# Kernel tuning notes

Hardware: AMD Instinct MI355X
Metric: run time of the kernel (lower is better)

Reference implementation:

```python
import jax, jax.numpy as jnp
import numpy as np

H, D, BLK, R = 12, 64, 64, 3  # heads, size_per_head, block size, rand blocks
NEG = -1e9


def setup_inputs() -> dict:
    key = jax.random.key(0)
    ks = jax.random.split(key, 6)
    B, S, W = 2, 4096, H * D
    M = S // BLK
    return {
        "from_tensor": jax.random.normal(ks[0], (B, S, W), jnp.float32),
        "to_tensor": jax.random.normal(ks[1], (B, S, W), jnp.float32),
        "Wq": jax.random.normal(ks[2], (W, H * D), jnp.float32) * 0.02,
        "bq": jnp.zeros((H * D,), jnp.float32),
        "Wk": jax.random.normal(ks[3], (W, H * D), jnp.float32) * 0.02,
        "bk": jnp.zeros((H * D,), jnp.float32),
        "Wv": jax.random.normal(ks[4], (W, H * D), jnp.float32) * 0.02,
        "bv": jnp.zeros((H * D,), jnp.float32),
        "to_mask": jnp.ones((B, S), jnp.int32),
        "rand_attn": jax.random.randint(ks[5], (H, M - 2, R), 0, M - 2, jnp.int32),
    }


def _bigbird_block_sparse(from_tensor, to_tensor, Wq, bq, Wk, bk, Wv, bv, to_mask, rand_attn):
    B, S, _ = from_tensor.shape
    M = S // BLK
    scale = 1.0 / np.sqrt(D).astype(np.float32)

    # QKV projections -> [B,H,S,D]
    q = (from_tensor @ Wq + bq).reshape(B, S, H, D).transpose(0, 2, 1, 3)
    k = (to_tensor @ Wk + bk).reshape(B, S, H, D).transpose(0, 2, 1, 3)
    v = (to_tensor @ Wv + bv).reshape(B, S, H, D).transpose(0, 2, 1, 3)

    bq_ = q.reshape(B, H, M, BLK, D)
    bk_ = k.reshape(B, H, M, BLK, D)
    bv_ = v.reshape(B, H, M, BLK, D)

    tm = to_mask.astype(q.dtype)          # [B,S]
    bm = tm.reshape(B, M, BLK)            # [B,M,BLK]

    # gather random key/value blocks per head: [B,H,M-2,R*BLK,D]
    ha = jnp.arange(H)[:, None, None]
    gk = bk_[:, ha, rand_attn].reshape(B, H, M - 2, R * BLK, D)
    gv = bv_[:, ha, rand_attn].reshape(B, H, M - 2, R * BLK, D)
    gm = bm[:, rand_attn].reshape(B, H, M - 2, R * BLK)

    def full_row(qblk):  # first/last query blocks attend to everything
        s = jnp.einsum('bhqd,bhkd->bhqk', qblk, k) * scale + (1 - tm)[:, None, None, :] * NEG
        return jnp.einsum('bhqk,bhkd->bhqd', jax.nn.softmax(s, -1), v)

    def sparse_row(qblk, k_cat, v_cat, m_cat):  # [B,H,BLK,D] x [B,H,L,D]
        s = jnp.einsum('bhqd,bhkd->bhqk', qblk, k_cat) * scale + (1 - m_cat)[:, :, None, :] * NEG
        return jnp.einsum('bhqk,bhkd->bhqd', jax.nn.softmax(s, -1), v_cat)

    c_first = full_row(bq_[:, :, 0])
    c_last = full_row(bq_[:, :, M - 1])

    # second row: blocks [0,1,2,last] + rand
    k2 = jnp.concatenate([bk_[:, :, 0], bk_[:, :, 1], bk_[:, :, 2], bk_[:, :, M - 1], gk[:, :, 0]], axis=2)
    v2 = jnp.concatenate([bv_[:, :, 0], bv_[:, :, 1], bv_[:, :, 2], bv_[:, :, M - 1], gv[:, :, 0]], axis=2)
    m2s = jnp.concatenate([bm[:, 0], bm[:, 1], bm[:, 2], bm[:, M - 1]], axis=-1)
    m2 = jnp.concatenate([jnp.broadcast_to(m2s[:, None], (B, H, 4 * BLK)), gm[:, :, 0]], axis=-1)
    c_second = sparse_row(bq_[:, :, 1], k2, v2, m2)

    # second-to-last row: blocks [0,M-3,M-2,M-1] + rand
    k3 = jnp.concatenate([bk_[:, :, 0], bk_[:, :, M - 3], bk_[:, :, M - 2], bk_[:, :, M - 1], gk[:, :, M - 3]], axis=2)
    v3 = jnp.concatenate([bv_[:, :, 0], bv_[:, :, M - 3], bv_[:, :, M - 2], bv_[:, :, M - 1], gv[:, :, M - 3]], axis=2)
    m3s = jnp.concatenate([bm[:, 0], bm[:, M - 3], bm[:, M - 2], bm[:, M - 1]], axis=-1)
    m3 = jnp.concatenate([jnp.broadcast_to(m3s[:, None], (B, H, 4 * BLK)), gm[:, :, M - 3]], axis=-1)
    c_secondlast = sparse_row(bq_[:, :, M - 2], k3, v3, m3)

    # middle rows 2..M-3: band(prev,self,next) + rand + global first/last blocks
    L = M - 4
    band_k = jnp.concatenate([bk_[:, :, 1:M - 3], bk_[:, :, 2:M - 2], bk_[:, :, 3:M - 1]], axis=3)  # [B,H,L,3BLK,D]
    band_v = jnp.concatenate([bv_[:, :, 1:M - 3], bv_[:, :, 2:M - 2], bv_[:, :, 3:M - 1]], axis=3)
    band_m = jnp.concatenate([bm[:, 1:M - 3], bm[:, 2:M - 2], bm[:, 3:M - 1]], axis=-1)  # [B,L,3BLK]

    k_mid = jnp.concatenate([
        band_k, gk[:, :, 1:M - 3],
        jnp.broadcast_to(bk_[:, :, 0:1], (B, H, L, BLK, D)),
        jnp.broadcast_to(bk_[:, :, M - 1:M], (B, H, L, BLK, D))], axis=3)
    v_mid = jnp.concatenate([
        band_v, gv[:, :, 1:M - 3],
        jnp.broadcast_to(bv_[:, :, 0:1], (B, H, L, BLK, D)),
        jnp.broadcast_to(bv_[:, :, M - 1:M], (B, H, L, BLK, D))], axis=3)
    m_mid = jnp.concatenate([
        jnp.broadcast_to(band_m[:, None], (B, H, L, 3 * BLK)),
        gm[:, :, 1:M - 3],
        jnp.broadcast_to(bm[:, None, None, 0], (B, H, L, BLK)),
        jnp.broadcast_to(bm[:, None, None, M - 1], (B, H, L, BLK))], axis=-1)

    s_mid = jnp.einsum('bhlqd,bhlkd->bhlqk', bq_[:, :, 2:M - 2], k_mid) * scale
    s_mid = s_mid + (1 - m_mid)[:, :, :, None, :] * NEG
    c_mid = jnp.einsum('bhlqk,bhlkd->bhlqd', jax.nn.softmax(s_mid, -1), v_mid)

    ctx = jnp.concatenate([
        c_first[:, :, None], c_second[:, :, None], c_mid,
        c_secondlast[:, :, None], c_last[:, :, None]], axis=2)  # [B,H,M,BLK,D]
    return ctx.reshape(B, H, S, D).transpose(0, 2, 1, 3)  # [B,S,H,D]


def reference(from_tensor, to_tensor, Wq, bq, Wk, bk, Wv, bv, to_mask, rand_attn):
    return _bigbird_block_sparse(from_tensor, to_tensor, Wq, bq, Wk, bk, Wv, bv, to_mask, rand_attn)
```

## Files before the change

kernel.cpp:

```cpp
#include <hip/hip_runtime.h>

typedef __attribute__((ext_vector_type(2))) float f32x2;
typedef __attribute__((ext_vector_type(4))) float f32x4;
typedef __attribute__((ext_vector_type(8))) __bf16 bf16x8;
typedef __attribute__((ext_vector_type(8))) unsigned short u16x8;
typedef __attribute__((ext_vector_type(4))) unsigned short u16x4;

#define LOG2E 1.4426950408889634f

__device__ __forceinline__ unsigned short f2bf(float f) {
  unsigned u = __builtin_bit_cast(unsigned, f);
  u += 0x7fffu + ((u >> 16) & 1u);
  return (unsigned short)(u >> 16);
}

__device__ __forceinline__ unsigned cvtpk(float lo, float hi) {
  unsigned r;
  asm("v_cvt_pk_bf16_f32 %0, %1, %2" : "=v"(r) : "v"(lo), "v"(hi));
  return r;
}

__device__ __forceinline__ f32x2 pkadd(f32x2 a, f32x2 b) {
  f32x2 r;
  asm("v_pk_add_f32 %0, %1, %2" : "=v"(r) : "v"(a), "v"(b));
  return r;
}

__device__ __forceinline__ float fexp2(float x) {
  float r;
  asm("v_exp_f32 %0, %1" : "=v"(r) : "v"(x));
  return r;
}

__device__ __forceinline__ f32x4 mfma16(bf16x8 a, bf16x8 b, f32x4 c) {
  return __builtin_amdgcn_mfma_f32_16x16x32_bf16(a, b, c, 0, 0, 0);
}

__device__ __forceinline__ void gload_lds16(const void* g, void* l) {
  __builtin_amdgcn_global_load_lds(
      (const __attribute__((address_space(1))) void*)g,
      (__attribute__((address_space(3))) void*)l, 16, 0, 0);
}

#define NQK 6291456
#define NX 6291456
#define NW 589824

__global__ __launch_bounds__(256) void prep_kernel(
    const float* __restrict__ Wq, const float* __restrict__ Wk,
    const float* __restrict__ Wv, const float* __restrict__ from_t,
    const float* __restrict__ to_t, unsigned short* __restrict__ Wt,
    unsigned short* __restrict__ xb) {
  __shared__ float tile[64][65];
  const int bid = blockIdx.x;
  const int t = threadIdx.x;
  if (bid < 432) {
    const int z = bid / 144, rest = bid % 144;
    const float* __restrict__ src = (z == 0) ? Wq : (z == 1) ? Wk : Wv;
    unsigned short* __restrict__ dst = Wt + (size_t)z * NW;
    const int k0 = (rest / 12) * 64, n0 = (rest % 12) * 64;
    const int r = t >> 4, c4 = (t & 15) * 4;
#pragma unroll
    for (int p = 0; p < 4; ++p) {
      int rr = r + p * 16;
      f32x4 v = *(const f32x4*)(src + (size_t)(k0 + rr) * 768 + n0 + c4);
#pragma unroll
      for (int j = 0; j < 4; ++j) tile[rr][c4 + j] = v[j];
    }
    __syncthreads();
#pragma unroll
    for (int p = 0; p < 4; ++p) {
      int rn = r + p * 16;
      u16x4 o;
#pragma unroll
      for (int j = 0; j < 4; ++j) o[j] = f2bf(tile[c4 + j][rn]);
      *(u16x4*)(dst + (size_t)(n0 + rn) * 768 + k0 + c4) = o;
    }
  } else {
    const int idx = bid - 432;
    const int y = idx / 3072, xi = idx % 3072;
    const float* __restrict__ src = y ? to_t : from_t;
    unsigned short* __restrict__ dst = xb + (size_t)y * NX;
    const size_t i = ((size_t)xi * 256 + t) * 8;
    f32x4 a = *(const f32x4*)(src + i);
    f32x4 b = *(const f32x4*)(src + i + 4);
    u16x8 o;
#pragma unroll
    for (int j = 0; j < 4; ++j) { o[j] = f2bf(a[j]); o[j + 4] = f2bf(b[j]); }
    *(u16x8*)(dst + i) = o;
  }
}

__global__ __launch_bounds__(256) void qkv_gemm_kernel(
    const unsigned short* __restrict__ Xb, const unsigned short* __restrict__ Wt,
    const float* __restrict__ bq, const float* __restrict__ bk,
    const float* __restrict__ bv, unsigned short* __restrict__ qkvQK,
    unsigned short* __restrict__ vt, int zoff, int cpx) {
  __shared__ unsigned short A_lds[2][8192];
  __shared__ unsigned short B_lds[2][8192];
  const int bid0 = blockIdx.x;
  const int bid = (bid0 & 7) * cpx + (bid0 >> 3);
  const int z = zoff + bid / 384;
  const int rem = bid % 384;
  const int bm = rem / 6, bn = rem % 6;
  const unsigned short* __restrict__ X = Xb + (z ? (size_t)NX : 0);
  const unsigned short* __restrict__ Wz = Wt + (size_t)z * NW;
  const float* __restrict__ bias = (z == 0) ? bq : (z == 1) ? bk : bv;
  const int t = threadIdx.x, lane = t & 63, w = t >> 6;
  const int wm = (w >> 1) * 64, wn = (w & 1) * 64;
  const int l15 = lane & 15, cc = lane >> 4;

  f32x4 acc[4][4];
#pragma unroll
  for (int i = 0; i < 4; ++i)
#pragma unroll
    for (int j = 0; j < 4; ++j) acc[i][j] = (f32x4){0.f, 0.f, 0.f, 0.f};

  const unsigned short* Abase = X + (size_t)bm * 128 * 768;
  const unsigned short* Bbase = Wz + (size_t)bn * 128 * 768;

  auto STAGE = [&](int ks, int bufi) {
#pragma unroll
    for (int p = 0; p < 4; ++p) {
      int wb = p * 4 + w;
      int ch = wb * 64 + lane;
      int r = ch >> 3, sl = ch & 7;
      int g = sl ^ (r & 7);
      gload_lds16(Abase + (size_t)r * 768 + ks * 64 + g * 8,
                  &A_lds[bufi][wb * 512]);
      gload_lds16(Bbase + (size_t)r * 768 + ks * 64 + g * 8,
                  &B_lds[bufi][wb * 512]);
    }
  };

  STAGE(0, 0);

  for (int ks = 0; ks < 12; ++ks) {
    const int cur = ks & 1;
    if (ks < 11) {
      STAGE(ks + 1, cur ^ 1);
      asm volatile("s_waitcnt vmcnt(8)" ::: "memory");
    } else {
      asm volatile("s_waitcnt vmcnt(0)" ::: "memory");
    }
    __builtin_amdgcn_s_barrier();
    __builtin_amdgcn_sched_barrier(0);

    bf16x8 af[4][2], bfr[4][2];
#pragma unroll
    for (int mi = 0; mi < 4; ++mi) {
      int row = wm + mi * 16 + l15;
      const char* rp = (const char*)A_lds[cur] + row * 128;
#pragma unroll
      for (int kk = 0; kk < 2; ++kk)
        af[mi][kk] = *(const bf16x8*)(rp + (((cc + 4 * kk) ^ (row & 7)) << 4));
    }
#pragma unroll
    for (int ni = 0; ni < 4; ++ni) {
      int row = wn + ni * 16 + l15;
      const char* rp = (const char*)B_lds[cur] + row * 128;
#pragma unroll
      for (int kk = 0; kk < 2; ++kk)
        bfr[ni][kk] = *(const bf16x8*)(rp + (((cc + 4 * kk) ^ (row & 7)) << 4));
    }
#pragma unroll
    for (int kk = 0; kk < 2; ++kk)
#pragma unroll
      for (int mi = 0; mi < 4; ++mi)
#pragma unroll
        for (int ni = 0; ni < 4; ++ni)
          acc[mi][ni] = mfma16(af[mi][kk], bfr[ni][kk], acc[mi][ni]);
    asm volatile("s_waitcnt lgkmcnt(0)" ::: "memory");
    __builtin_amdgcn_s_barrier();
  }

  if (z < 2) {
    const float qscale = (z == 0) ? 0.125f * LOG2E : 1.0f;
    unsigned short* __restrict__ dst = qkvQK + (size_t)z * NQK;
#pragma unroll
    for (int ni = 0; ni < 4; ++ni) {
      int gn = bn * 128 + wn + ni * 16 + l15;
      float bv_ = bias[gn];
      int hh = gn >> 6, dd = gn & 63;
#pragma unroll
      for (int mi = 0; mi < 4; ++mi) {
#pragma unroll
        for (int r = 0; r < 4; ++r) {
          int gm = bm * 128 + wm + mi * 16 + cc * 4 + r;
          int bb = gm >> 12, s = gm & 4095;
          float val = (acc[mi][ni][r] + bv_) * qscale;
          dst[((((size_t)bb * 12 + hh) * 4096 + s) * 64) + dd] = f2bf(val);
        }
      }
    }
  } else {
#pragma unroll
    for (int ni = 0; ni < 4; ++ni) {
      int gn = bn * 128 + wn + ni * 16 + l15;
      float bv_ = bias[gn];
      int hh = gn >> 6, dd = gn & 63;
#pragma unroll
      for (int mi = 0; mi < 4; ++mi) {
        int gm0 = bm * 128 + wm + mi * 16 + cc * 4;
        int bb = gm0 >> 12, s0 = gm0 & 4095;
        u16x4 o;
#pragma unroll
        for (int r = 0; r < 4; ++r) o[r] = f2bf(acc[mi][ni][r] + bv_);
        *(u16x4*)(vt + ((size_t)(bb * 12 + hh) * 64 + dd) * 4096 + s0) = o;
      }
    }
  }
}

__global__ __launch_bounds__(256, 4) void attn_kernel(
    const unsigned short* __restrict__ qkvQK, const unsigned short* __restrict__ vt,
    const int* __restrict__ to_mask, const int* __restrict__ rand_attn,
    float* __restrict__ out, float* __restrict__ part_o,
    float* __restrict__ part_ml) {
  __shared__ unsigned short K_lds[2][4096];
  __shared__ unsigned short VT_lds[2][4096];
  __shared__ float penal[8][64];
  __shared__ int blist[8];

  const int bid0 = blockIdx.x;
  const int bid = (bid0 & 7) * 234 + (bid0 >> 3);
  const int bh = bid / 78, r78 = bid % 78;
  const int h = bh % 12, b = bh / 12;
  const int t = threadIdx.x, lane = t & 63, w = t >> 6;
  const int l15 = lane & 15, cc = lane >> 4;

  int m, nblk, chunk = 0;
  bool full;
  if (r78 < 62) {
    full = false;
    m = r78 + 1;
    nblk = (m == 1 || m == 62) ? 7 : 8;
    if (t == 0) {
      const int* rp = rand_attn + ((size_t)h * 62 + (m - 1)) * 3;
      if (m == 1) {
        blist[0] = 0; blist[1] = 1; blist[2] = 2; blist[3] = 63;
        blist[4] = rp[0]; blist[5] = rp[1]; blist[6] = rp[2];
      } else if (m == 62) {
        blist[0] = 0; blist[1] = 61; blist[2] = 62; blist[3] = 63;
        blist[4] = rp[0]; blist[5] = rp[1]; blist[6] = rp[2];
      } else {
        blist[0] = m - 1; blist[1] = m; blist[2] = m + 1;
        blist[3] = rp[0]; blist[4] = rp[1]; blist[5] = rp[2];
        blist[6] = 0; blist[7] = 63;
      }
    }
  } else {
    full = true;
    int fr = r78 - 62;
    chunk = fr & 7;
    m = (fr >> 3) ? 63 : 0;
    nblk = 8;
    if (t < 8) blist[t] = chunk * 8 + t;
  }

  const unsigned short* qp = qkvQK + (((size_t)b * 12 + h) * 4096 + m * 64) * 64;
  const unsigned short* kp = qkvQK + NQK + (((size_t)b * 12 + h) * 4096) * 64;
  const unsigned short* vtp = vt + (((size_t)b * 12 + h) * 64) * 4096;

  int loff[2];
  const unsigned short *kpl[2], *vpl[2];
#pragma unroll
  for (int p = 0; p < 2; ++p) {
    int wb = p * 4 + w;
    int ch = wb * 64 + lane;
    int rr = ch >> 3;
    int g = (ch & 7) ^ (rr & 7);
    loff[p] = wb * 512;
    kpl[p] = kp + rr * 64 + g * 8;
    vpl[p] = vtp + rr * 4096 + g * 8;
  }

  int vaddr[4];
#pragma unroll
  for (int dg = 0; dg < 4; ++dg) {
    int d = dg * 16 + l15;
    vaddr[dg] = d * 128 + ((((cc >> 1) ^ (d & 7)) << 4)) + (cc & 1) * 8;
  }

  bf16x8 aq[2];
  {
    int qrow = w * 16 + l15;
    aq[0] = *(const bf16x8*)(qp + qrow * 64 + cc * 8);
    aq[1] = *(const bf16x8*)(qp + qrow * 64 + 32 + cc * 8);
  }

  float m_run = -INFINITY, l_run = 0.f;
  f32x4 o_acc[4];
#pragma unroll
  for (int dg = 0; dg < 4; ++dg) o_acc[dg] = (f32x4){0.f, 0.f, 0.f, 0.f};

  auto STAGE_K = [&](int kb, int bufi) {
    const size_t ko = (size_t)kb * 4096;
    gload_lds16(kpl[0] + ko, &K_lds[bufi][loff[0]]);
    gload_lds16(kpl[1] + ko, &K_lds[bufi][loff[1]]);
  };
  auto STAGE_V = [&](int kb, int bufi) {
    const size_t vo = (size_t)kb * 64;
    gload_lds16(vpl[0] + vo, &VT_lds[bufi][loff[0]]);
    gload_lds16(vpl[1] + vo, &VT_lds[bufi][loff[1]]);
  };

  auto QK = [&](int bufi, int slot, float s[4][4]) {
    const char* kbase = (const char*)K_lds[bufi];
    __builtin_amdgcn_s_setprio(1);
#pragma unroll
    for (int kg = 0; kg < 4; ++kg) {
      int krow = kg * 16 + l15;
      const char* rp = kbase + krow * 128;
      int sz = (krow & 7) << 4;
      bf16x8 k0 = *(const bf16x8*)(rp + ((cc << 4) ^ sz));
      bf16x8 k1 = *(const bf16x8*)(rp + (((cc + 4) << 4) ^ sz));
      f32x4 pen = *(const f32x4*)(&penal[slot][kg * 16 + cc * 4]);
      f32x4 zz = mfma16(k0, aq[0], pen);
      zz = mfma16(k1, aq[1], zz);
#pragma unroll
      for (int r = 0; r < 4; ++r) s[kg][r] = zz[r];
    }
    __builtin_amdgcn_s_setprio(0);
  };

  __syncthreads();

  {
    int ib = w;
#pragma unroll
    for (int pp = 0; pp < 2; ++pp, ib += 4)
      if (ib < nblk)
        penal[ib][lane] =
            (1.0f - (float)to_mask[(size_t)b * 4096 + blist[ib] * 64 + lane]) *
            (-1e9f * LOG2E);
  }
  STAGE_K(blist[0], 0);
  STAGE_V(blist[0], 0);
  STAGE_K(blist[1], 1);
  asm volatile("s_waitcnt vmcnt(4) lgkmcnt(0)" ::: "memory");
  __builtin_amdgcn_s_barrier();
  __builtin_amdgcn_sched_barrier(0);

  float sm[4][4];
  QK(0, 0, sm);

  union PF { unsigned u[4]; bf16x8 v; };
  union VF { u16x4 h2[2]; bf16x8 v; };

  for (int ib = 0; ib < nblk; ++ib) {
    asm volatile("s_waitcnt vmcnt(0)" ::: "memory");
    __builtin_amdgcn_s_barrier();
    __builtin_amdgcn_sched_barrier(0);

    if (ib + 2 < nblk) STAGE_K(blist[ib + 2], ib & 1);
    if (ib + 1 < nblk) STAGE_V(blist[ib + 1], (ib + 1) & 1);

    float sn[4][4];
    if (ib + 1 < nblk) QK((ib + 1) & 1, ib + 1, sn);

    float m1 = fmaxf(fmaxf(sm[0][0], sm[0][1]), sm[0][2]);
    float m2 = fmaxf(fmaxf(sm[0][3], sm[1][0]), sm[1][1]);
    float m3 = fmaxf(fmaxf(sm[1][2], sm[1][3]), sm[2][0]);
    float m4 = fmaxf(fmaxf(sm[2][1], sm[2][2]), sm[2][3]);
    float m5 = fmaxf(fmaxf(sm[3][0], sm[3][1]), sm[3][2]);
    float mx = fmaxf(fmaxf(fmaxf(m1, m2), m3),
                     fmaxf(fmaxf(m4, m5), sm[3][3]));
    mx = fmaxf(mx, __shfl_xor(mx, 16, 64));
    mx = fmaxf(mx, __shfl_xor(mx, 32, 64));

    if (!__all(mx - m_run <= 8.0f)) {
      float mn = fmaxf(m_run, mx);
      float fac = fexp2(m_run - mn);
      m_run = mn;
      l_run *= fac;
      float fr_[4];
#pragma unroll
      for (int r = 0; r < 4; ++r) fr_[r] = __shfl(fac, cc * 4 + r, 64);
#pragma unroll
      for (int dg = 0; dg < 4; ++dg)
#pragma unroll
        for (int r = 0; r < 4; ++r) o_acc[dg][r] *= fr_[r];
    }

    unsigned pk[8];
    f32x2 ps[8];
#pragma unroll
    for (int kg = 0; kg < 4; ++kg) {
      float p0 = fexp2(sm[kg][0] - m_run), p1 = fexp2(sm[kg][1] - m_run);
      float p2 = fexp2(sm[kg][2] - m_run), p3 = fexp2(sm[kg][3] - m_run);
      pk[kg * 2] = cvtpk(p0, p1);
      pk[kg * 2 + 1] = cvtpk(p2, p3);
      ps[kg * 2] = (f32x2){p0, p1};
      ps[kg * 2 + 1] = (f32x2){p2, p3};
    }
    f32x2 s0 = pkadd(pkadd(ps[0], ps[1]), pkadd(ps[2], ps[3]));
    f32x2 s1 = pkadd(pkadd(ps[4], ps[5]), pkadd(ps[6], ps[7]));
    f32x2 st = pkadd(s0, s1);
    float rs = st[0] + st[1];
    rs += __shfl_xor(rs, 16, 64);
    rs += __shfl_xor(rs, 32, 64);
    l_run += rs;

    PF a0, a1;
    a0.u[0] = pk[0]; a0.u[1] = pk[1]; a0.u[2] = pk[2]; a0.u[3] = pk[3];
    a1.u[0] = pk[4]; a1.u[1] = pk[5]; a1.u[2] = pk[6]; a1.u[3] = pk[7];

    const char* vbuf = (const char*)VT_lds[ib & 1];
    __builtin_amdgcn_s_setprio(1);
#pragma unroll
    for (int dg = 0; dg < 4; ++dg) {
      int a00 = vaddr[dg];
      VF f0, f1;
      f0.h2[0] = *(const u16x4*)(vbuf + a00);
      f0.h2[1] = *(const u16x4*)(vbuf + (a00 ^ 32));
      f1.h2[0] = *(const u16x4*)(vbuf + (a00 ^ 64));
      f1.h2[1] = *(const u16x4*)(vbuf + (a00 ^ 96));
      o_acc[dg] = mfma16(a0.v, f0.v, o_acc[dg]);
      o_acc[dg] = mfma16(a1.v, f1.v, o_acc[dg]);
    }
    __builtin_amdgcn_s_setprio(0);

    if (ib + 1 < nblk) {
#pragma unroll
      for (int kg = 0; kg < 4; ++kg)
#pragma unroll
        for (int r = 0; r < 4; ++r) sm[kg][r] = sn[kg][r];
    }
  }

  if (!full) {
    float inv[4];
#pragma unroll
    for (int r = 0; r < 4; ++r) inv[r] = 1.0f / __shfl(l_run, cc * 4 + r, 64);
#pragma unroll
    for (int r = 0; r < 4; ++r) {
      int s = m * 64 + w * 16 + cc * 4 + r;
#pragma unroll
      for (int dg = 0; dg < 4; ++dg) {
        int d = dg * 16 + l15;
        out[(((size_t)b * 4096 + s) * 12 + h) * 64 + d] = o_acc[dg][r] * inv[r];
      }
    }
  } else {
    const int row = (b * 12 + h) * 2 + (m ? 1 : 0);
    float* po = part_o + (((size_t)row * 8 + chunk) * 64) * 64;
    float* pml = part_ml + ((size_t)row * 8 + chunk) * 128;
#pragma unroll
    for (int r = 0; r < 4; ++r) {
      int q = w * 16 + cc * 4 + r;
#pragma unroll
      for (int dg = 0; dg < 4; ++dg) {
        int d = dg * 16 + l15;
        po[q * 64 + d] = o_acc[dg][r];
      }
    }
    if (cc == 0) {
      pml[w * 16 + l15] = m_run;
      pml[64 + w * 16 + l15] = l_run;
    }
  }
}

__global__ __launch_bounds__(256) void combine_kernel(
    const float* __restrict__ part_o, const float* __restrict__ part_ml,
    float* __restrict__ out) {
  const int row = blockIdx.x;
  const int b = row / 24, h = (row >> 1) % 12, m = (row & 1) ? 63 : 0;
  const int t = threadIdx.x;
  const int q = t >> 2, d0 = (t & 3) * 16;

  float mc[8], lc[8];
  float M = -INFINITY;
#pragma unroll
  for (int c = 0; c < 8; ++c) {
    const float* pml = part_ml + ((size_t)row * 8 + c) * 128;
    mc[c] = pml[q];
    lc[c] = pml[64 + q];
    M = fmaxf(M, mc[c]);
  }
  float wgt[8], L = 0.f;
#pragma unroll
  for (int c = 0; c < 8; ++c) {
    float r;
    asm("v_exp_f32 %0, %1" : "=v"(r) : "v"(mc[c] - M));
    wgt[c] = r;
    L += wgt[c] * lc[c];
  }
  f32x4 acc[4];
#pragma unroll
  for (int j = 0; j < 4; ++j) acc[j] = (f32x4){0.f, 0.f, 0.f, 0.f};
#pragma unroll
  for (int c = 0; c < 8; ++c) {
    const float* po = part_o + (((size_t)row * 8 + c) * 64 + q) * 64 + d0;
#pragma unroll
    for (int j = 0; j < 4; ++j) {
      f32x4 v = *(const f32x4*)(po + j * 4);
#pragma unroll
      for (int e = 0; e < 4; ++e) acc[j][e] += wgt[c] * v[e];
    }
  }
  const float inv = 1.0f / L;
  const int s = m * 64 + q;
  float* op = out + (((size_t)b * 4096 + s) * 12 + h) * 64 + d0;
#pragma unroll
  for (int j = 0; j < 4; ++j) {
    f32x4 v;
#pragma unroll
    for (int e = 0; e < 4; ++e) v[e] = acc[j][e] * inv;
    *(f32x4*)(op + j * 4) = v;
  }
}

extern "C" void kernel_launch(void* const* d_in, const int* in_sizes, int n_in,
                              void* d_out, int out_size, void* d_ws,
                              size_t ws_size, hipStream_t stream) {
  (void)in_sizes; (void)n_in; (void)out_size;
  const float* from_t = (const float*)d_in[0];
  const float* to_t = (const float*)d_in[1];
  const float* Wq = (const float*)d_in[2];
  const float* bq = (const float*)d_in[3];
  const float* Wk = (const float*)d_in[4];
  const float* bk = (const float*)d_in[5];
  const float* Wv = (const float*)d_in[6];
  const float* bv = (const float*)d_in[7];
  const int* to_mask = (const int*)d_in[8];
  const int* rand_attn = (const int*)d_in[9];
  float* out = (float*)d_out;

  unsigned short* Wt = (unsigned short*)d_ws;
  unsigned short* qkvQK = Wt + (size_t)3 * NW;
  unsigned short* Xb = qkvQK + (size_t)2 * NQK;

  const size_t part_elems = (size_t)48 * 8 * 64 * 64 + (size_t)48 * 8 * 128;
  const size_t fused_bytes =
      ((size_t)3 * NW + 2 * NQK + 2 * NX + NQK) * 2 + part_elems * 4;

  if (ws_size >= fused_bytes) {
    unsigned short* vt = Xb + (size_t)2 * NX;
    float* part_o = (float*)Xb;
    float* part_ml = part_o + (size_t)48 * 8 * 64 * 64;

    prep_kernel<<<dim3(6576), dim3(256), 0, stream>>>(Wq, Wk, Wv, from_t, to_t,
                                                      Wt, Xb);
    qkv_gemm_kernel<<<dim3(1152), dim3(256), 0, stream>>>(
        Xb, Wt, bq, bk, bv, qkvQK, vt, 0, 144);
    attn_kernel<<<dim3(1872), dim3(256), 0, stream>>>(
        qkvQK, vt, to_mask, rand_attn, out, part_o, part_ml);
    combine_kernel<<<dim3(48), dim3(256), 0, stream>>>(part_o, part_ml, out);
  } else {
    unsigned short* vt = Xb;
    float* part_o = (float*)(Xb + (size_t)NX);
    float* part_ml = part_o + (size_t)48 * 8 * 64 * 64;

    prep_kernel<<<dim3(6576), dim3(256), 0, stream>>>(Wq, Wk, Wv, from_t, to_t,
                                                      Wt, Xb);
    qkv_gemm_kernel<<<dim3(768), dim3(256), 0, stream>>>(
        Xb, Wt, bq, bk, bv, qkvQK, vt, 0, 96);
    qkv_gemm_kernel<<<dim3(384), dim3(256), 0, stream>>>(
        Xb, Wt, bq, bk, bv, qkvQK, vt, 2, 48);
    attn_kernel<<<dim3(1872), dim3(256), 0, stream>>>(
        qkvQK, vt, to_mask, rand_attn, out, part_o, part_ml);
    combine_kernel<<<dim3(48), dim3(256), 0, stream>>>(part_o, part_ml, out);
  }
}
```

Before: 101.7 us.

## Fuse fp32-to-bf16 activation conversion into QKV GEMM A-tile loading

The separate prep pass that converted from/to tensors to bf16 in workspace is removed. The GEMM now loads fp32 activation rows into registers, converts them with packed bf16 conversion and writes them swizzled into LDS, while B tiles still use direct global-to-LDS loads. This removes a full write and re-read of the bf16 activation copies and drops the two-launch fallback path. In exchange, the GEMM reads twice as many bytes for A per tile, uses more registers and needs a more complex wait schedule.

```diff
diff --git a/kernel.cpp b/kernel.cpp
--- a/kernel.cpp
+++ b/kernel.cpp
@@ -5,6 +5,7 @@
 typedef __attribute__((ext_vector_type(8))) __bf16 bf16x8;
 typedef __attribute__((ext_vector_type(8))) unsigned short u16x8;
 typedef __attribute__((ext_vector_type(4))) unsigned short u16x4;
+typedef __attribute__((ext_vector_type(4))) unsigned int u32x4;
 
 #define LOG2E 1.4426950408889634f
 
@@ -43,67 +44,51 @@
 }
 
 #define NQK 6291456
-#define NX 6291456
 #define NW 589824
 
 __global__ __launch_bounds__(256) void prep_kernel(
     const float* __restrict__ Wq, const float* __restrict__ Wk,
-    const float* __restrict__ Wv, const float* __restrict__ from_t,
-    const float* __restrict__ to_t, unsigned short* __restrict__ Wt,
-    unsigned short* __restrict__ xb) {
+    const float* __restrict__ Wv, unsigned short* __restrict__ Wt) {
   __shared__ float tile[64][65];
   const int bid = blockIdx.x;
   const int t = threadIdx.x;
-  if (bid < 432) {
-    const int z = bid / 144, rest = bid % 144;
-    const float* __restrict__ src = (z == 0) ? Wq : (z == 1) ? Wk : Wv;
-    unsigned short* __restrict__ dst = Wt + (size_t)z * NW;
-    const int k0 = (rest / 12) * 64, n0 = (rest % 12) * 64;
-    const int r = t >> 4, c4 = (t & 15) * 4;
-#pragma unroll
-    for (int p = 0; p < 4; ++p) {
-      int rr = r + p * 16;
-      f32x4 v = *(const f32x4*)(src + (size_t)(k0 + rr) * 768 + n0 + c4);
-#pragma unroll
-      for (int j = 0; j < 4; ++j) tile[rr][c4 + j] = v[j];
-    }
-    __syncthreads();
-#pragma unroll
-    for (int p = 0; p < 4; ++p) {
-      int rn = r + p * 16;
-      u16x4 o;
-#pragma unroll
-      for (int j = 0; j < 4; ++j) o[j] = f2bf(tile[c4 + j][rn]);
-      *(u16x4*)(dst + (size_t)(n0 + rn) * 768 + k0 + c4) = o;
-    }
-  } else {
-    const int idx = bid - 432;
-    const int y = idx / 3072, xi = idx % 3072;
-    const float* __restrict__ src = y ? to_t : from_t;
-    unsigned short* __restrict__ dst = xb + (size_t)y * NX;
-    const size_t i = ((size_t)xi * 256 + t) * 8;
-    f32x4 a = *(const f32x4*)(src + i);
-    f32x4 b = *(const f32x4*)(src + i + 4);
-    u16x8 o;
-#pragma unroll
-    for (int j = 0; j < 4; ++j) { o[j] = f2bf(a[j]); o[j + 4] = f2bf(b[j]); }
-    *(u16x8*)(dst + i) = o;
+  const int z = bid / 144, rest = bid % 144;
+  const float* __restrict__ src = (z == 0) ? Wq : (z == 1) ? Wk : Wv;
+  unsigned short* __restrict__ dst = Wt + (size_t)z * NW;
+  const int k0 = (rest / 12) * 64, n0 = (rest % 12) * 64;
+  const int r = t >> 4, c4 = (t & 15) * 4;
+#pragma unroll
+  for (int p = 0; p < 4; ++p) {
+    int rr = r + p * 16;
+    f32x4 v = *(const f32x4*)(src + (size_t)(k0 + rr) * 768 + n0 + c4);
+#pragma unroll
+    for (int j = 0; j < 4; ++j) tile[rr][c4 + j] = v[j];
+  }
+  __syncthreads();
+#pragma unroll
+  for (int p = 0; p < 4; ++p) {
+    int rn = r + p * 16;
+    u16x4 o;
+#pragma unroll
+    for (int j = 0; j < 4; ++j) o[j] = f2bf(tile[c4 + j][rn]);
+    *(u16x4*)(dst + (size_t)(n0 + rn) * 768 + k0 + c4) = o;
   }
 }
 
 __global__ __launch_bounds__(256) void qkv_gemm_kernel(
-    const unsigned short* __restrict__ Xb, const unsigned short* __restrict__ Wt,
+    const float* __restrict__ from_t, const float* __restrict__ to_t,
+    const unsigned short* __restrict__ Wt,
     const float* __restrict__ bq, const float* __restrict__ bk,
     const float* __restrict__ bv, unsigned short* __restrict__ qkvQK,
-    unsigned short* __restrict__ vt, int zoff, int cpx) {
+    unsigned short* __restrict__ vt) {
   __shared__ unsigned short A_lds[2][8192];
   __shared__ unsigned short B_lds[2][8192];
   const int bid0 = blockIdx.x;
-  const int bid = (bid0 & 7) * cpx + (bid0 >> 3);
-  const int z = zoff + bid / 384;
+  const int bid = (bid0 & 7) * 144 + (bid0 >> 3);
+  const int z = bid / 384;
   const int rem = bid % 384;
   const int bm = rem / 6, bn = rem % 6;
-  const unsigned short* __restrict__ X = Xb + (z ? (size_t)NX : 0);
+  const float* __restrict__ X = z ? to_t : from_t;
   const unsigned short* __restrict__ Wz = Wt + (size_t)z * NW;
   const float* __restrict__ bias = (z == 0) ? bq : (z == 1) ? bk : bv;
   const int t = threadIdx.x, lane = t & 63, w = t >> 6;
@@ -116,32 +101,57 @@
 #pragma unroll
     for (int j = 0; j < 4; ++j) acc[i][j] = (f32x4){0.f, 0.f, 0.f, 0.f};
 
-  const unsigned short* Abase = X + (size_t)bm * 128 * 768;
   const unsigned short* Bbase = Wz + (size_t)bn * 128 * 768;
 
-  auto STAGE = [&](int ks, int bufi) {
+  const int g_ = (t & 7) ^ ((t >> 3) & 7);
+  const float* arow0 = X + (size_t)(bm * 128 + (t >> 3)) * 768 + g_ * 8;
+
+  auto LOAD_A = [&](int ks, f32x4* av) {
+#pragma unroll
+    for (int p = 0; p < 4; ++p) {
+      const float* pp = arow0 + (size_t)p * 32 * 768 + ks * 64;
+      av[2 * p] = *(const f32x4*)pp;
+      av[2 * p + 1] = *(const f32x4*)(pp + 4);
+    }
+  };
+  auto WRITE_A = [&](int bufi, const f32x4* av) {
+    char* dst = (char*)A_lds[bufi] + t * 16;
+#pragma unroll
+    for (int p = 0; p < 4; ++p) {
+      u32x4 wv;
+      wv[0] = cvtpk(av[2 * p][0], av[2 * p][1]);
+      wv[1] = cvtpk(av[2 * p][2], av[2 * p][3]);
+      wv[2] = cvtpk(av[2 * p + 1][0], av[2 * p + 1][1]);
+      wv[3] = cvtpk(av[2 * p + 1][2], av[2 * p + 1][3]);
+      *(u32x4*)(dst + p * 4096) = wv;
+    }
+  };
+  auto STAGE_B = [&](int ks, int bufi) {
 #pragma unroll
     for (int p = 0; p < 4; ++p) {
       int wb = p * 4 + w;
       int ch = wb * 64 + lane;
       int r = ch >> 3, sl = ch & 7;
       int g = sl ^ (r & 7);
-      gload_lds16(Abase + (size_t)r * 768 + ks * 64 + g * 8,
-                  &A_lds[bufi][wb * 512]);
       gload_lds16(Bbase + (size_t)r * 768 + ks * 64 + g * 8,
                   &B_lds[bufi][wb * 512]);
     }
   };
 
-  STAGE(0, 0);
+  f32x4 av[8];
+  LOAD_A(0, av);
+  STAGE_B(0, 0);
+  asm volatile("s_waitcnt vmcnt(4)" ::: "memory");
+  WRITE_A(0, av);
 
   for (int ks = 0; ks < 12; ++ks) {
     const int cur = ks & 1;
     if (ks < 11) {
-      STAGE(ks + 1, cur ^ 1);
-      asm volatile("s_waitcnt vmcnt(8)" ::: "memory");
+      LOAD_A(ks + 1, av);
+      STAGE_B(ks + 1, cur ^ 1);
+      asm volatile("s_waitcnt vmcnt(12) lgkmcnt(0)" ::: "memory");
     } else {
-      asm volatile("s_waitcnt vmcnt(0)" ::: "memory");
+      asm volatile("s_waitcnt vmcnt(0) lgkmcnt(0)" ::: "memory");
     }
     __builtin_amdgcn_s_barrier();
     __builtin_amdgcn_sched_barrier(0);
@@ -170,8 +180,13 @@
 #pragma unroll
         for (int ni = 0; ni < 4; ++ni)
           acc[mi][ni] = mfma16(af[mi][kk], bfr[ni][kk], acc[mi][ni]);
-    asm volatile("s_waitcnt lgkmcnt(0)" ::: "memory");
-    __builtin_amdgcn_s_barrier();
+
+    if (ks < 11) {
+      asm volatile("s_waitcnt vmcnt(4)" ::: "memory");
+      WRITE_A(cur ^ 1, av);
+      asm volatile("s_waitcnt lgkmcnt(0)" ::: "memory");
+      __builtin_amdgcn_s_barrier();
+    }
   }
 
   if (z < 2) {
@@ -482,9 +497,7 @@
   float wgt[8], L = 0.f;
 #pragma unroll
   for (int c = 0; c < 8; ++c) {
-    float r;
-    asm("v_exp_f32 %0, %1" : "=v"(r) : "v"(mc[c] - M));
-    wgt[c] = r;
+    wgt[c] = fexp2(mc[c] - M);
     L += wgt[c] * lc[c];
   }
   f32x4 acc[4];
@@ -515,7 +528,7 @@
 extern "C" void kernel_launch(void* const* d_in, const int* in_sizes, int n_in,
                               void* d_out, int out_size, void* d_ws,
                               size_t ws_size, hipStream_t stream) {
-  (void)in_sizes; (void)n_in; (void)out_size;
+  (void)in_sizes; (void)n_in; (void)out_size; (void)ws_size;
   const float* from_t = (const float*)d_in[0];
   const float* to_t = (const float*)d_in[1];
   const float* Wq = (const float*)d_in[2];
@@ -530,37 +543,14 @@
 
   unsigned short* Wt = (unsigned short*)d_ws;
   unsigned short* qkvQK = Wt + (size_t)3 * NW;
-  unsigned short* Xb = qkvQK + (size_t)2 * NQK;
-
-  const size_t part_elems = (size_t)48 * 8 * 64 * 64 + (size_t)48 * 8 * 128;
-  const size_t fused_bytes =
-      ((size_t)3 * NW + 2 * NQK + 2 * NX + NQK) * 2 + part_elems * 4;
-
-  if (ws_size >= fused_bytes) {
-    unsigned short* vt = Xb + (size_t)2 * NX;
-    float* part_o = (float*)Xb;
-    float* part_ml = part_o + (size_t)48 * 8 * 64 * 64;
-
-    prep_kernel<<<dim3(6576), dim3(256), 0, stream>>>(Wq, Wk, Wv, from_t, to_t,
-                                                      Wt, Xb);
-    qkv_gemm_kernel<<<dim3(1152), dim3(256), 0, stream>>>(
-        Xb, Wt, bq, bk, bv, qkvQK, vt, 0, 144);
-    attn_kernel<<<dim3(1872), dim3(256), 0, stream>>>(
-        qkvQK, vt, to_mask, rand_attn, out, part_o, part_ml);
-    combine_kernel<<<dim3(48), dim3(256), 0, stream>>>(part_o, part_ml, out);
-  } else {
-    unsigned short* vt = Xb;
-    float* part_o = (float*)(Xb + (size_t)NX);
-    float* part_ml = part_o + (size_t)48 * 8 * 64 * 64;
-
-    prep_kernel<<<dim3(6576), dim3(256), 0, stream>>>(Wq, Wk, Wv, from_t, to_t,
-                                                      Wt, Xb);
-    qkv_gemm_kernel<<<dim3(768), dim3(256), 0, stream>>>(
-        Xb, Wt, bq, bk, bv, qkvQK, vt, 0, 96);
-    qkv_gemm_kernel<<<dim3(384), dim3(256), 0, stream>>>(
-        Xb, Wt, bq, bk, bv, qkvQK, vt, 2, 48);
-    attn_kernel<<<dim3(1872), dim3(256), 0, stream>>>(
-        qkvQK, vt, to_mask, rand_attn, out, part_o, part_ml);
-    combine_kernel<<<dim3(48), dim3(256), 0, stream>>>(part_o, part_ml, out);
-  }
-}
+  unsigned short* vt = qkvQK + (size_t)2 * NQK;
+  float* part_o = (float*)(vt + (size_t)NQK);
+  float* part_ml = part_o + (size_t)48 * 8 * 64 * 64;
+
+  prep_kernel<<<dim3(432), dim3(256), 0, stream>>>(Wq, Wk, Wv, Wt);
+  qkv_gemm_kernel<<<dim3(1152), dim3(256), 0, stream>>>(
+      from_t, to_t, Wt, bq, bk, bv, qkvQK, vt);
+  attn_kernel<<<dim3(1872), dim3(256), 0, stream>>>(
+      qkvQK, vt, to_mask, rand_attn, out, part_o, part_ml);
+  combine_kernel<<<dim3(48), dim3(256), 0, stream>>>(part_o, part_ml, out);
+}
```

After: 110.9 us. 9.0% more time.
